# Kernel tuning notes

Hardware: AMD Instinct MI355X
Metric: run time of the kernel (lower is better)

Reference implementation:

```python
import jax, jax.numpy as jnp
import numpy as np

N = 50000      # nodes
E = 800000     # edges (avg degree 16)
IN = 256       # input feature dim
H = 4          # heads
F = 64         # out_feats per head
EF = 64        # edge_feats
NT = 8         # num_etypes
SLOPE = 0.2    # leaky relu negative slope


def setup_inputs() -> dict:
    key = jax.random.key(0)
    ks = jax.random.split(key, 10)
    return {
        "nfeat": jax.random.normal(ks[0], (N, IN), dtype=jnp.float32),
        "fc_w": jax.random.normal(ks[1], (IN, H * F), dtype=jnp.float32) * 0.05,
        "fc_e_w": jax.random.normal(ks[2], (EF, H * EF), dtype=jnp.float32) * 0.05,
        "attn_l": jax.random.normal(ks[3], (H, F), dtype=jnp.float32) * 0.1,
        "attn_r": jax.random.normal(ks[4], (H, F), dtype=jnp.float32) * 0.1,
        "attn_e": jax.random.normal(ks[5], (H, EF), dtype=jnp.float32) * 0.1,
        "edge_emb": jax.random.normal(ks[6], (NT, EF), dtype=jnp.float32),
        "src": jax.random.randint(ks[7], (E,), 0, N, dtype=jnp.int32),
        "dst": jax.random.randint(ks[8], (E,), 0, N, dtype=jnp.int32),
        "etype": jax.random.randint(ks[9], (E,), 0, NT, dtype=jnp.int32),
    }


def reference(nfeat, fc_w, fc_e_w, attn_l, attn_r, attn_e, edge_emb, src, dst, etype):
    # node projection: [N, H, F]
    feat = (nfeat @ fc_w).reshape(N, H, F)
    # per-node attention halves: [N, H]
    el = jnp.einsum("nhf,hf->nh", feat, attn_l)
    er = jnp.einsum("nhf,hf->nh", feat, attn_r)
    # per-etype edge attention term: fc_e(edge_emb).view(NT,H,EF) . attn_e -> [NT, H]
    e_feat = (edge_emb @ fc_e_w).reshape(NT, H, EF)
    ee = jnp.einsum("the,he->th", e_feat, attn_e)
    # raw edge scores: [E, H]
    e = el[src] + er[dst] + ee[etype]
    a_raw = jax.nn.leaky_relu(e, negative_slope=SLOPE)
    # edge_softmax over destination nodes (homogeneous graph -> all edges together)
    seg_max = jax.ops.segment_max(a_raw, dst, num_segments=N)  # [N, H]
    a_exp = jnp.exp(a_raw - seg_max[dst])
    seg_sum = jax.ops.segment_sum(a_exp, dst, num_segments=N)  # [N, H]
    a = a_exp / seg_sum[dst]                                   # [E, H]
    # weighted gather-sum aggregation: sum_e a[e] * feat[src[e]] per dst
    msg = feat[src] * a[:, :, None]                            # [E, H, F]
    rst = jax.ops.segment_sum(msg, dst, num_segments=N)        # [N, H, F]
    return rst, a
```

## Files before the change

kernel.cpp:

```cpp
#include <hip/hip_runtime.h>

#define N_NODES 50000
#define E_EDGES 800000
#define IN_DIM 256
#define H_HEADS 4
#define F_OUT 64
#define EF_DIM 64
#define NT_TYPES 8
#define SLOPE 0.2f
#define HF 256

typedef __attribute__((ext_vector_type(8))) short short8;
typedef __attribute__((ext_vector_type(4))) float f32x4;
typedef unsigned short ushort_t;
typedef unsigned long long u64;

#define FEATBF_OFF 0
#define EL_OFF   6400000
#define ER_OFF   6600000
#define EE_OFF   6800000
#define BT_OFF   6800064
#define INT_OFF  6832832
#define DEG_IOFF     0
#define CURSOR_IOFF  50000
#define RL_IOFF      100000
#define PK_IOFF      150008
#define BO_IOFF      1750008

#define NBLK_GEMM 782
#define NBLK_HIST 3125
#define NCHUNK    196

__device__ __forceinline__ ushort_t f2bf(float f) {
    unsigned u = __float_as_uint(f);
    u += 0x7fffu + ((u >> 16) & 1u);
    return (ushort_t)(u >> 16);
}
__device__ __forceinline__ float bf2f(ushort_t b) {
    return __uint_as_float(((unsigned)b) << 16);
}

__global__ __launch_bounds__(256) void k1_prep(
    const float* __restrict__ edge_emb, const float* __restrict__ fc_e_w,
    const float* __restrict__ attn_e, const float* __restrict__ fc_w,
    float* __restrict__ ee, ushort_t* __restrict__ Bt, int* __restrict__ zero_region)
{
    const int b = blockIdx.x;
    if (b == 0) {
        const int c = threadIdx.x;
        const float ae = attn_e[c];
        const int lane = c & 63, h = c >> 6;
        for (int ty = 0; ty < NT_TYPES; ty++) {
            float v = 0.f;
            #pragma unroll 8
            for (int k = 0; k < EF_DIM; k++)
                v = fmaf(edge_emb[ty * EF_DIM + k], fc_e_w[k * (H_HEADS * EF_DIM) + c], v);
            float contrib = v * ae;
            #pragma unroll
            for (int m = 32; m >= 1; m >>= 1) contrib += __shfl_xor(contrib, m);
            if (lane == 0) ee[ty * H_HEADS + h] = contrib;
        }
    } else if (b <= 256) {
        const int k = b - 1, c = threadIdx.x;
        Bt[(size_t)c * 256 + k] = f2bf(fc_w[(size_t)k * 256 + c]);
    } else {
        const int idx = (b - 257) * 256 + threadIdx.x;
        if (idx < 2 * N_NODES) zero_region[idx] = 0;
    }
}

__global__ __launch_bounds__(256) void k2_hist(
    const int* __restrict__ dst, int* __restrict__ deg)
{
    const int t = blockIdx.x * 256 + threadIdx.x;
    if (t < E_EDGES) atomicAdd(deg + dst[t], 1);
}

__global__ __launch_bounds__(256) void scanA(
    const int* __restrict__ deg, int* __restrict__ rl, int* __restrict__ bo)
{
    __shared__ int sm[256];
    const int c = blockIdx.x, t = threadIdx.x;
    const int g = c * 256 + t;
    const int v = (g < N_NODES) ? deg[g] : 0;
    sm[t] = v;
    __syncthreads();
    int val = v;
    #pragma unroll
    for (int o = 1; o < 256; o <<= 1) {
        int x = (t >= o) ? sm[t - o] : 0;
        __syncthreads();
        val += x;
        sm[t] = val;
        __syncthreads();
    }
    if (g < N_NODES) rl[g] = val - v;
    if (t == 255) bo[c] = val;
}

__global__ __launch_bounds__(256) void scanB(int* __restrict__ bo)
{
    __shared__ int sm[256];
    const int t = threadIdx.x;
    const int v = (t < NCHUNK) ? bo[t] : 0;
    sm[t] = v;
    __syncthreads();
    int val = v;
    #pragma unroll
    for (int o = 1; o < 256; o <<= 1) {
        int x = (t >= o) ? sm[t - o] : 0;
        __syncthreads();
        val += x;
        sm[t] = val;
        __syncthreads();
    }
    if (t < NCHUNK) bo[t] = val - v;
}

__device__ __forceinline__ void gemm_body(
    const float* __restrict__ nfeat, const ushort_t* __restrict__ Bt,
    const float* __restrict__ attn_l, const float* __restrict__ attn_r,
    ushort_t* __restrict__ feat, float* __restrict__ el, float* __restrict__ er,
    int blk)
{
    const int w    = threadIdx.x >> 6;
    const int lane = threadIdx.x & 63;
    const int n16  = lane & 15;
    const int quad = lane >> 4;
    const int row0 = blk * 64;

    f32x4 acc[4][4];
    #pragma unroll
    for (int rt = 0; rt < 4; rt++)
        #pragma unroll
        for (int ct = 0; ct < 4; ct++)
            acc[rt][ct] = (f32x4){0.f, 0.f, 0.f, 0.f};

    for (int kb = 0; kb < IN_DIM; kb += 32) {
        short8 a[4], b[4];
        #pragma unroll
        for (int rt = 0; rt < 4; rt++) {
            int r = row0 + rt * 16 + n16;
            r = r < N_NODES ? r : N_NODES - 1;
            const float* p = nfeat + (size_t)r * IN_DIM + kb + quad * 8;
            const float4 v0 = *(const float4*)p;
            const float4 v1 = *(const float4*)(p + 4);
            short8 t;
            t[0] = (short)f2bf(v0.x); t[1] = (short)f2bf(v0.y);
            t[2] = (short)f2bf(v0.z); t[3] = (short)f2bf(v0.w);
            t[4] = (short)f2bf(v1.x); t[5] = (short)f2bf(v1.y);
            t[6] = (short)f2bf(v1.z); t[7] = (short)f2bf(v1.w);
            a[rt] = t;
        }
        #pragma unroll
        for (int ct = 0; ct < 4; ct++) {
            const int c = w * 64 + ct * 16 + n16;
            b[ct] = *(const short8*)(Bt + (size_t)c * 256 + kb + quad * 8);
        }
        #pragma unroll
        for (int rt = 0; rt < 4; rt++)
            #pragma unroll
            for (int ct = 0; ct < 4; ct++)
                acc[rt][ct] = __builtin_amdgcn_mfma_f32_16x16x32_bf16(a[rt], b[ct], acc[rt][ct], 0, 0, 0);
    }

    float alv[4], arv[4];
    #pragma unroll
    for (int ct = 0; ct < 4; ct++) {
        alv[ct] = attn_l[w * 64 + ct * 16 + n16];
        arv[ct] = attn_r[w * 64 + ct * 16 + n16];
    }
    #pragma unroll
    for (int rt = 0; rt < 4; rt++) {
        #pragma unroll
        for (int reg = 0; reg < 4; reg++) {
            const int row = row0 + rt * 16 + quad * 4 + reg;
            const bool ok = row < N_NODES;
            float pl = 0.f, pr = 0.f;
            #pragma unroll
            for (int ct = 0; ct < 4; ct++) {
                const float v = acc[rt][ct][reg];
                if (ok) feat[(size_t)row * HF + w * 64 + ct * 16 + n16] = f2bf(v);
                pl = fmaf(v, alv[ct], pl);
                pr = fmaf(v, arv[ct], pr);
            }
            #pragma unroll
            for (int m = 8; m >= 1; m >>= 1) {
                pl += __shfl_xor(pl, m);
                pr += __shfl_xor(pr, m);
            }
            if (n16 == 0 && ok) {
                el[row * H_HEADS + w] = pl;
                er[row * H_HEADS + w] = pr;
            }
        }
    }
}

__global__ __launch_bounds__(256) void k4_gemm_scatter(
    const float* __restrict__ nfeat, const ushort_t* __restrict__ Bt,
    const float* __restrict__ attn_l, const float* __restrict__ attn_r,
    ushort_t* __restrict__ feat, float* __restrict__ el, float* __restrict__ er,
    const int* __restrict__ src, const int* __restrict__ dst, const int* __restrict__ etype,
    const int* __restrict__ rl, const int* __restrict__ bo,
    int* __restrict__ cursor, u64* __restrict__ pk)
{
    if (blockIdx.x < NBLK_GEMM) {
        gemm_body(nfeat, Bt, attn_l, attn_r, feat, el, er, blockIdx.x);
    } else {
        const int t = (blockIdx.x - NBLK_GEMM) * 256 + threadIdx.x;
        if (t < E_EDGES) {
            const int d = dst[t];
            const int pos = bo[d >> 8] + rl[d] + atomicAdd(cursor + d, 1);
            pk[pos] = (u64)src[t] | ((u64)etype[t] << 16) | ((u64)t << 32);
        }
    }
}

__global__ __launch_bounds__(256) void agg_kernel(
    const u64* __restrict__ pk, const int* __restrict__ rl, const int* __restrict__ bo,
    const int* __restrict__ degarr,
    const float* __restrict__ el, const float* __restrict__ er,
    const float* __restrict__ ee, const ushort_t* __restrict__ feat,
    float* __restrict__ a_out, float* __restrict__ rst)
{
    const int d = blockIdx.x;
    const int t = threadIdx.x;
    const int h = t >> 6, lane = t & 63;
    const int off = bo[d >> 8] + rl[d];
    const int deg = degarr[d];

    __shared__ int sS[256];
    __shared__ int sE[256];
    __shared__ float sc[4][256];

    if (deg <= 248) {
        const int degP = (deg + 15) & ~15;
        if (t < deg) {
            const u64 p = pk[off + t];
            const int s  = (int)(p & 0xffffu);
            const int ty = (int)((p >> 16) & 0xffu);
            sS[t] = s;
            sE[t] = (int)(p >> 32);
            const float4 el4 = *(const float4*)(el + s * 4);
            const float4 er4 = *(const float4*)(er + d * 4);
            const float4 ee4 = *(const float4*)(ee + ty * 4);
            float v;
            v = el4.x + er4.x + ee4.x; sc[0][t] = v > 0.f ? v : SLOPE * v;
            v = el4.y + er4.y + ee4.y; sc[1][t] = v > 0.f ? v : SLOPE * v;
            v = el4.z + er4.z + ee4.z; sc[2][t] = v > 0.f ? v : SLOPE * v;
            v = el4.w + er4.w + ee4.w; sc[3][t] = v > 0.f ? v : SLOPE * v;
        } else if (t < degP) {
            sS[t] = 0;
            sc[0][t] = 0.f; sc[1][t] = 0.f; sc[2][t] = 0.f; sc[3][t] = 0.f;
        }
        __syncthreads();

        float m = -INFINITY;
        for (int i = lane; i < deg; i += 64) m = fmaxf(m, sc[h][i]);
        #pragma unroll
        for (int w = 32; w >= 1; w >>= 1) m = fmaxf(m, __shfl_xor(m, w));

        float s = 0.f;
        for (int i = lane; i < deg; i += 64) {
            const float e = __expf(sc[h][i] - m);
            sc[h][i] = e;
            s += e;
        }
        #pragma unroll
        for (int w = 32; w >= 1; w >>= 1) s += __shfl_xor(s, w);
        const float inv = 1.f / s;

        for (int i = lane; i < deg; i += 64) {
            const float a = sc[h][i] * inv;
            sc[h][i] = a;
            a_out[sE[i] * 4 + h] = a;
        }
        __syncthreads();

        const int q   = lane >> 4;
        const int l16 = lane & 15;
        const uint2* fb = (const uint2*)feat;
        float a0 = 0.f, a1 = 0.f, a2 = 0.f, a3 = 0.f;
        for (int i = 0; i < degP; i += 16) {
            int sn[4]; float aw[4];
            #pragma unroll
            for (int j = 0; j < 4; j++) {
                const int idx = i + j * 4 + q;
                sn[j] = sS[idx];
                aw[j] = sc[h][idx];
            }
            uint2 u[4];
            #pragma unroll
            for (int j = 0; j < 4; j++)
                u[j] = fb[(size_t)sn[j] * 64 + h * 16 + l16];
            #pragma unroll
            for (int j = 0; j < 4; j++) {
                a0 = fmaf(aw[j], __uint_as_float(u[j].x << 16),          a0);
                a1 = fmaf(aw[j], __uint_as_float(u[j].x & 0xffff0000u),  a1);
                a2 = fmaf(aw[j], __uint_as_float(u[j].y << 16),          a2);
                a3 = fmaf(aw[j], __uint_as_float(u[j].y & 0xffff0000u),  a3);
            }
        }
        a0 += __shfl_xor(a0, 16); a0 += __shfl_xor(a0, 32);
        a1 += __shfl_xor(a1, 16); a1 += __shfl_xor(a1, 32);
        a2 += __shfl_xor(a2, 16); a2 += __shfl_xor(a2, 32);
        a3 += __shfl_xor(a3, 16); a3 += __shfl_xor(a3, 32);
        if (q == 0) {
            float4 o = {a0, a1, a2, a3};
            *(float4*)(rst + (size_t)d * HF + h * 64 + l16 * 4) = o;
        }
    } else {
        const float erh = er[d * 4 + h];
        float m = -INFINITY;
        for (int i = lane; i < deg; i += 64) {
            const u64 p = pk[off + i];
            float v = el[(int)(p & 0xffffu) * 4 + h] + erh + ee[(int)((p >> 16) & 0xffu) * 4 + h];
            v = v > 0.f ? v : SLOPE * v;
            m = fmaxf(m, v);
        }
        #pragma unroll
        for (int w = 32; w >= 1; w >>= 1) m = fmaxf(m, __shfl_xor(m, w));
        float s = 0.f;
        for (int i = lane; i < deg; i += 64) {
            const u64 p = pk[off + i];
            float v = el[(int)(p & 0xffffu) * 4 + h] + erh + ee[(int)((p >> 16) & 0xffu) * 4 + h];
            v = v > 0.f ? v : SLOPE * v;
            s += __expf(v - m);
        }
        #pragma unroll
        for (int w = 32; w >= 1; w >>= 1) s += __shfl_xor(s, w);
        const float inv = 1.f / s;
        float acc = 0.f;
        for (int i = 0; i < deg; i++) {
            const u64 p = pk[off + i];
            const int sn = (int)(p & 0xffffu);
            float v = el[sn * 4 + h] + erh + ee[(int)((p >> 16) & 0xffu) * 4 + h];
            v = v > 0.f ? v : SLOPE * v;
            const float a = __expf(v - m) * inv;
            if (lane == 0) a_out[(int)(p >> 32) * 4 + h] = a;
            acc = fmaf(a, bf2f(feat[(size_t)sn * HF + h * 64 + lane]), acc);
        }
        rst[(size_t)d * HF + h * 64 + lane] = acc;
    }
}

extern "C" void kernel_launch(void* const* d_in, const int* in_sizes, int n_in,
                              void* d_out, int out_size, void* d_ws, size_t ws_size,
                              hipStream_t stream) {
    const float* nfeat    = (const float*)d_in[0];
    const float* fc_w     = (const float*)d_in[1];
    const float* fc_e_w   = (const float*)d_in[2];
    const float* attn_l   = (const float*)d_in[3];
    const float* attn_r   = (const float*)d_in[4];
    const float* attn_e   = (const float*)d_in[5];
    const float* edge_emb = (const float*)d_in[6];
    const int*   src      = (const int*)d_in[7];
    const int*   dst      = (const int*)d_in[8];
    const int*   etype    = (const int*)d_in[9];

    float* ws = (float*)d_ws;
    ushort_t* feat = (ushort_t*)(ws + FEATBF_OFF);
    float* el   = ws + EL_OFF;
    float* er   = ws + ER_OFF;
    float* ee   = ws + EE_OFF;
    ushort_t* Bt = (ushort_t*)(ws + BT_OFF);
    int*   ip      = (int*)(ws + INT_OFF);
    int*   deg     = ip + DEG_IOFF;
    int*   cursor  = ip + CURSOR_IOFF;
    int*   rl      = ip + RL_IOFF;
    u64*   pk      = (u64*)(ip + PK_IOFF);
    int*   bo      = ip + BO_IOFF;

    float* rst   = (float*)d_out;
    float* a_out = (float*)d_out + (size_t)N_NODES * HF;

    k1_prep<<<648, 256, 0, stream>>>(edge_emb, fc_e_w, attn_e, fc_w, ee, Bt, deg);
    k2_hist<<<NBLK_HIST, 256, 0, stream>>>(dst, deg);
    scanA<<<NCHUNK, 256, 0, stream>>>(deg, rl, bo);
    scanB<<<1, 256, 0, stream>>>(bo);
    k4_gemm_scatter<<<NBLK_GEMM + NBLK_HIST, 256, 0, stream>>>(
        nfeat, Bt, attn_l, attn_r, feat, el, er,
        src, dst, etype, rl, bo, cursor, pk);
    agg_kernel<<<N_NODES, 256, 0, stream>>>(pk, rl, bo, deg, el, er, ee, feat, a_out, rst);
}
```

Before: 335.7 us.

## Spread GEMM blocks across CSR-build kernels and use one wave per node in aggregation

The 782 GEMM tiles are split across the histogram, both scan and scatter kernels so projection work overlaps with the serial CSR-building stages. The histogram and scatter now read int4 vectors, handling four edges per thread. Aggregation maps one 64-lane wave per destination node (16 lanes per head) instead of a 256-thread block, and normalisation is deferred to the end. This removes block-level barriers and the idle threads seen at low degree, at the cost of more complex kernel partitioning and LDS use of about 20KB per block.

```diff
diff --git a/kernel.cpp b/kernel.cpp
--- a/kernel.cpp
+++ b/kernel.cpp
@@ -28,8 +28,17 @@
 #define BO_IOFF      1750008
 
 #define NBLK_GEMM 782
-#define NBLK_HIST 3125
+#define NBLK_E4   782
 #define NCHUNK    196
+
+#define G2   312
+#define G3A  120
+#define G3B  100
+#define G4   250
+#define G2_BASE   0
+#define G3A_BASE  312
+#define G3B_BASE  432
+#define G4_BASE   532
 
 __device__ __forceinline__ ushort_t f2bf(float f) {
     unsigned u = __float_as_uint(f);
@@ -69,54 +78,6 @@
     }
 }
 
-__global__ __launch_bounds__(256) void k2_hist(
-    const int* __restrict__ dst, int* __restrict__ deg)
-{
-    const int t = blockIdx.x * 256 + threadIdx.x;
-    if (t < E_EDGES) atomicAdd(deg + dst[t], 1);
-}
-
-__global__ __launch_bounds__(256) void scanA(
-    const int* __restrict__ deg, int* __restrict__ rl, int* __restrict__ bo)
-{
-    __shared__ int sm[256];
-    const int c = blockIdx.x, t = threadIdx.x;
-    const int g = c * 256 + t;
-    const int v = (g < N_NODES) ? deg[g] : 0;
-    sm[t] = v;
-    __syncthreads();
-    int val = v;
-    #pragma unroll
-    for (int o = 1; o < 256; o <<= 1) {
-        int x = (t >= o) ? sm[t - o] : 0;
-        __syncthreads();
-        val += x;
-        sm[t] = val;
-        __syncthreads();
-    }
-    if (g < N_NODES) rl[g] = val - v;
-    if (t == 255) bo[c] = val;
-}
-
-__global__ __launch_bounds__(256) void scanB(int* __restrict__ bo)
-{
-    __shared__ int sm[256];
-    const int t = threadIdx.x;
-    const int v = (t < NCHUNK) ? bo[t] : 0;
-    sm[t] = v;
-    __syncthreads();
-    int val = v;
-    #pragma unroll
-    for (int o = 1; o < 256; o <<= 1) {
-        int x = (t >= o) ? sm[t - o] : 0;
-        __syncthreads();
-        val += x;
-        sm[t] = val;
-        __syncthreads();
-    }
-    if (t < NCHUNK) bo[t] = val - v;
-}
-
 __device__ __forceinline__ void gemm_body(
     const float* __restrict__ nfeat, const ushort_t* __restrict__ Bt,
     const float* __restrict__ attn_l, const float* __restrict__ attn_r,
@@ -197,7 +158,86 @@
     }
 }
 
-__global__ __launch_bounds__(256) void k4_gemm_scatter(
+__global__ __launch_bounds__(256) void k2_hist_gemm(
+    const float* __restrict__ nfeat, const ushort_t* __restrict__ Bt,
+    const float* __restrict__ attn_l, const float* __restrict__ attn_r,
+    ushort_t* __restrict__ feat, float* __restrict__ el, float* __restrict__ er,
+    const int* __restrict__ dst, int* __restrict__ deg)
+{
+    if (blockIdx.x < NBLK_E4) {
+        const int t = blockIdx.x * 256 + threadIdx.x;
+        if (t < E_EDGES / 4) {
+            const int4 d4 = ((const int4*)dst)[t];
+            atomicAdd(deg + d4.x, 1);
+            atomicAdd(deg + d4.y, 1);
+            atomicAdd(deg + d4.z, 1);
+            atomicAdd(deg + d4.w, 1);
+        }
+    } else {
+        gemm_body(nfeat, Bt, attn_l, attn_r, feat, el, er,
+                  G2_BASE + (int)blockIdx.x - NBLK_E4);
+    }
+}
+
+__global__ __launch_bounds__(256) void scanA_gemm(
+    const float* __restrict__ nfeat, const ushort_t* __restrict__ Bt,
+    const float* __restrict__ attn_l, const float* __restrict__ attn_r,
+    ushort_t* __restrict__ feat, float* __restrict__ el, float* __restrict__ er,
+    const int* __restrict__ deg, int* __restrict__ rl, int* __restrict__ bo)
+{
+    if (blockIdx.x < NCHUNK) {
+        __shared__ int sm[256];
+        const int c = blockIdx.x, t = threadIdx.x;
+        const int g = c * 256 + t;
+        const int v = (g < N_NODES) ? deg[g] : 0;
+        sm[t] = v;
+        __syncthreads();
+        int val = v;
+        #pragma unroll
+        for (int o = 1; o < 256; o <<= 1) {
+            int x = (t >= o) ? sm[t - o] : 0;
+            __syncthreads();
+            val += x;
+            sm[t] = val;
+            __syncthreads();
+        }
+        if (g < N_NODES) rl[g] = val - v;
+        if (t == 255) bo[c] = val;
+    } else {
+        gemm_body(nfeat, Bt, attn_l, attn_r, feat, el, er,
+                  G3A_BASE + (int)blockIdx.x - NCHUNK);
+    }
+}
+
+__global__ __launch_bounds__(256) void scanB_gemm(
+    const float* __restrict__ nfeat, const ushort_t* __restrict__ Bt,
+    const float* __restrict__ attn_l, const float* __restrict__ attn_r,
+    ushort_t* __restrict__ feat, float* __restrict__ el, float* __restrict__ er,
+    int* __restrict__ bo)
+{
+    if (blockIdx.x == 0) {
+        __shared__ int sm[256];
+        const int t = threadIdx.x;
+        const int v = (t < NCHUNK) ? bo[t] : 0;
+        sm[t] = v;
+        __syncthreads();
+        int val = v;
+        #pragma unroll
+        for (int o = 1; o < 256; o <<= 1) {
+            int x = (t >= o) ? sm[t - o] : 0;
+            __syncthreads();
+            val += x;
+            sm[t] = val;
+            __syncthreads();
+        }
+        if (t < NCHUNK) bo[t] = val - v;
+    } else {
+        gemm_body(nfeat, Bt, attn_l, attn_r, feat, el, er,
+                  G3B_BASE + (int)blockIdx.x - 1);
+    }
+}
+
+__global__ __launch_bounds__(256) void k4_scatter_gemm(
     const float* __restrict__ nfeat, const ushort_t* __restrict__ Bt,
     const float* __restrict__ attn_l, const float* __restrict__ attn_r,
     ushort_t* __restrict__ feat, float* __restrict__ el, float* __restrict__ er,
@@ -205,15 +245,26 @@
     const int* __restrict__ rl, const int* __restrict__ bo,
     int* __restrict__ cursor, u64* __restrict__ pk)
 {
-    if (blockIdx.x < NBLK_GEMM) {
-        gemm_body(nfeat, Bt, attn_l, attn_r, feat, el, er, blockIdx.x);
-    } else {
-        const int t = (blockIdx.x - NBLK_GEMM) * 256 + threadIdx.x;
-        if (t < E_EDGES) {
-            const int d = dst[t];
-            const int pos = bo[d >> 8] + rl[d] + atomicAdd(cursor + d, 1);
-            pk[pos] = (u64)src[t] | ((u64)etype[t] << 16) | ((u64)t << 32);
-        }
+    if (blockIdx.x < NBLK_E4) {
+        const int t = blockIdx.x * 256 + threadIdx.x;
+        if (t < E_EDGES / 4) {
+            const int4 s4 = ((const int4*)src)[t];
+            const int4 d4 = ((const int4*)dst)[t];
+            const int4 e4 = ((const int4*)etype)[t];
+            const int eb = t * 4;
+            int pos;
+            pos = bo[d4.x >> 8] + rl[d4.x] + atomicAdd(cursor + d4.x, 1);
+            pk[pos] = (u64)s4.x | ((u64)e4.x << 16) | ((u64)(eb + 0) << 32);
+            pos = bo[d4.y >> 8] + rl[d4.y] + atomicAdd(cursor + d4.y, 1);
+            pk[pos] = (u64)s4.y | ((u64)e4.y << 16) | ((u64)(eb + 1) << 32);
+            pos = bo[d4.z >> 8] + rl[d4.z] + atomicAdd(cursor + d4.z, 1);
+            pk[pos] = (u64)s4.z | ((u64)e4.z << 16) | ((u64)(eb + 2) << 32);
+            pos = bo[d4.w >> 8] + rl[d4.w] + atomicAdd(cursor + d4.w, 1);
+            pk[pos] = (u64)s4.w | ((u64)e4.w << 16) | ((u64)(eb + 3) << 32);
+        }
+    } else {
+        gemm_body(nfeat, Bt, attn_l, attn_r, feat, el, er,
+                  G4_BASE + (int)blockIdx.x - NBLK_E4);
     }
 }
 
@@ -224,124 +275,150 @@
     const float* __restrict__ ee, const ushort_t* __restrict__ feat,
     float* __restrict__ a_out, float* __restrict__ rst)
 {
-    const int d = blockIdx.x;
-    const int t = threadIdx.x;
-    const int h = t >> 6, lane = t & 63;
+    const int wid  = threadIdx.x >> 6;
+    const int d    = blockIdx.x * 4 + wid;
+    const int lane = threadIdx.x & 63;
+    const int h    = lane >> 4;
+    const int l    = lane & 15;
+
+    __shared__ __align__(16) ushort_t sS[4][256];
+    __shared__ __align__(16) float    aB[4][256 * 4];
+
+    if (d >= N_NODES) return;
+    ushort_t* sSw = sS[wid];
+    float*    aBw = aB[wid];
+    const uint2* fb = (const uint2*)feat;
+
     const int off = bo[d >> 8] + rl[d];
     const int deg = degarr[d];
-
-    __shared__ int sS[256];
-    __shared__ int sE[256];
-    __shared__ float sc[4][256];
-
-    if (deg <= 248) {
-        const int degP = (deg + 15) & ~15;
-        if (t < deg) {
-            const u64 p = pk[off + t];
-            const int s  = (int)(p & 0xffffu);
-            const int ty = (int)((p >> 16) & 0xffu);
-            sS[t] = s;
-            sE[t] = (int)(p >> 32);
-            const float4 el4 = *(const float4*)(el + s * 4);
-            const float4 er4 = *(const float4*)(er + d * 4);
-            const float4 ee4 = *(const float4*)(ee + ty * 4);
-            float v;
-            v = el4.x + er4.x + ee4.x; sc[0][t] = v > 0.f ? v : SLOPE * v;
-            v = el4.y + er4.y + ee4.y; sc[1][t] = v > 0.f ? v : SLOPE * v;
-            v = el4.z + er4.z + ee4.z; sc[2][t] = v > 0.f ? v : SLOPE * v;
-            v = el4.w + er4.w + ee4.w; sc[3][t] = v > 0.f ? v : SLOPE * v;
-        } else if (t < degP) {
-            sS[t] = 0;
-            sc[0][t] = 0.f; sc[1][t] = 0.f; sc[2][t] = 0.f; sc[3][t] = 0.f;
-        }
-        __syncthreads();
+    const float erh = er[d * 4 + h];
+
+    if (deg <= 256) {
+        const int nch  = (deg + 15) >> 4;
+        const int degP = nch << 4;
 
         float m = -INFINITY;
-        for (int i = lane; i < deg; i += 64) m = fmaxf(m, sc[h][i]);
-        #pragma unroll
-        for (int w = 32; w >= 1; w >>= 1) m = fmaxf(m, __shfl_xor(m, w));
+        for (int c = 0; c < nch; c++) {
+            const int e = c * 16 + l;
+            float v = -INFINITY;
+            if (e < deg) {
+                const u64 p = pk[off + e];
+                const int s  = (int)(p & 0xffffu);
+                const int ty = (int)((p >> 16) & 0xffu);
+                if (h == 0) sSw[e] = (ushort_t)s;
+                v = el[s * 4 + h] + erh + ee[ty * 4 + h];
+                v = v > 0.f ? v : SLOPE * v;
+                aBw[e * 4 + h] = v;
+            }
+            m = fmaxf(m, v);
+        }
+        m = fmaxf(m, __shfl_xor(m, 1));
+        m = fmaxf(m, __shfl_xor(m, 2));
+        m = fmaxf(m, __shfl_xor(m, 4));
+        m = fmaxf(m, __shfl_xor(m, 8));
 
         float s = 0.f;
-        for (int i = lane; i < deg; i += 64) {
-            const float e = __expf(sc[h][i] - m);
-            sc[h][i] = e;
-            s += e;
-        }
-        #pragma unroll
-        for (int w = 32; w >= 1; w >>= 1) s += __shfl_xor(s, w);
-        const float inv = 1.f / s;
-
-        for (int i = lane; i < deg; i += 64) {
-            const float a = sc[h][i] * inv;
-            sc[h][i] = a;
-            a_out[sE[i] * 4 + h] = a;
-        }
-        __syncthreads();
-
-        const int q   = lane >> 4;
-        const int l16 = lane & 15;
-        const uint2* fb = (const uint2*)feat;
-        float a0 = 0.f, a1 = 0.f, a2 = 0.f, a3 = 0.f;
-        for (int i = 0; i < degP; i += 16) {
-            int sn[4]; float aw[4];
+        for (int c = 0; c < nch; c++) {
+            const int e = c * 16 + l;
+            float ev = 0.f;
+            if (e < deg) ev = __expf(aBw[e * 4 + h] - m);
+            else if (h == 0) sSw[e] = 0;
+            aBw[e * 4 + h] = ev;
+            s += ev;
+        }
+        s += __shfl_xor(s, 1);
+        s += __shfl_xor(s, 2);
+        s += __shfl_xor(s, 4);
+        s += __shfl_xor(s, 8);
+        const float inv = (deg > 0) ? 1.f / s : 0.f;
+
+        asm volatile("s_waitcnt lgkmcnt(0)" ::: "memory");
+
+        const float inv0 = __shfl(inv, 0);
+        const float inv1 = __shfl(inv, 16);
+        const float inv2 = __shfl(inv, 32);
+        const float inv3 = __shfl(inv, 48);
+
+        if (h == 0) {
+            for (int c = 0; c < nch; c++) {
+                const int e = c * 16 + l;
+                if (e < deg) {
+                    const u64 p = pk[off + e];
+                    const int eid = (int)(p >> 32);
+                    const float4 t = *(const float4*)(aBw + e * 4);
+                    float4 av;
+                    av.x = t.x * inv0;
+                    av.y = t.y * inv1;
+                    av.z = t.z * inv2;
+                    av.w = t.w * inv3;
+                    *(float4*)(a_out + (size_t)eid * 4) = av;
+                }
+            }
+        }
+
+        float4 acc = {0.f, 0.f, 0.f, 0.f};
+        const int col = h * 16 + l;
+        for (int e0 = 0; e0 < degP; e0 += 4) {
             #pragma unroll
             for (int j = 0; j < 4; j++) {
-                const int idx = i + j * 4 + q;
-                sn[j] = sS[idx];
-                aw[j] = sc[h][idx];
-            }
-            uint2 u[4];
-            #pragma unroll
-            for (int j = 0; j < 4; j++)
-                u[j] = fb[(size_t)sn[j] * 64 + h * 16 + l16];
-            #pragma unroll
-            for (int j = 0; j < 4; j++) {
-                a0 = fmaf(aw[j], __uint_as_float(u[j].x << 16),          a0);
-                a1 = fmaf(aw[j], __uint_as_float(u[j].x & 0xffff0000u),  a1);
-                a2 = fmaf(aw[j], __uint_as_float(u[j].y << 16),          a2);
-                a3 = fmaf(aw[j], __uint_as_float(u[j].y & 0xffff0000u),  a3);
-            }
-        }
-        a0 += __shfl_xor(a0, 16); a0 += __shfl_xor(a0, 32);
-        a1 += __shfl_xor(a1, 16); a1 += __shfl_xor(a1, 32);
-        a2 += __shfl_xor(a2, 16); a2 += __shfl_xor(a2, 32);
-        a3 += __shfl_xor(a3, 16); a3 += __shfl_xor(a3, 32);
-        if (q == 0) {
-            float4 o = {a0, a1, a2, a3};
-            *(float4*)(rst + (size_t)d * HF + h * 64 + l16 * 4) = o;
-        }
-    } else {
-        const float erh = er[d * 4 + h];
+                const int e = e0 + j;
+                const int sn = (int)sSw[e];
+                const float aw = aBw[e * 4 + h];
+                const uint2 u = fb[(size_t)sn * 64 + col];
+                acc.x = fmaf(aw, __uint_as_float(u.x << 16),         acc.x);
+                acc.y = fmaf(aw, __uint_as_float(u.x & 0xffff0000u), acc.y);
+                acc.z = fmaf(aw, __uint_as_float(u.y << 16),         acc.z);
+                acc.w = fmaf(aw, __uint_as_float(u.y & 0xffff0000u), acc.w);
+            }
+        }
+        acc.x *= inv; acc.y *= inv; acc.z *= inv; acc.w *= inv;
+        *(float4*)(rst + (size_t)d * HF + h * 64 + l * 4) = acc;
+    } else {
         float m = -INFINITY;
-        for (int i = lane; i < deg; i += 64) {
+        for (int i = l; i < deg; i += 16) {
             const u64 p = pk[off + i];
             float v = el[(int)(p & 0xffffu) * 4 + h] + erh + ee[(int)((p >> 16) & 0xffu) * 4 + h];
             v = v > 0.f ? v : SLOPE * v;
             m = fmaxf(m, v);
         }
-        #pragma unroll
-        for (int w = 32; w >= 1; w >>= 1) m = fmaxf(m, __shfl_xor(m, w));
+        m = fmaxf(m, __shfl_xor(m, 1));
+        m = fmaxf(m, __shfl_xor(m, 2));
+        m = fmaxf(m, __shfl_xor(m, 4));
+        m = fmaxf(m, __shfl_xor(m, 8));
         float s = 0.f;
-        for (int i = lane; i < deg; i += 64) {
+        for (int i = l; i < deg; i += 16) {
             const u64 p = pk[off + i];
             float v = el[(int)(p & 0xffffu) * 4 + h] + erh + ee[(int)((p >> 16) & 0xffu) * 4 + h];
             v = v > 0.f ? v : SLOPE * v;
             s += __expf(v - m);
         }
-        #pragma unroll
-        for (int w = 32; w >= 1; w >>= 1) s += __shfl_xor(s, w);
+        s += __shfl_xor(s, 1);
+        s += __shfl_xor(s, 2);
+        s += __shfl_xor(s, 4);
+        s += __shfl_xor(s, 8);
         const float inv = 1.f / s;
-        float acc = 0.f;
-        for (int i = 0; i < deg; i++) {
+        for (int i = l; i < deg; i += 16) {
             const u64 p = pk[off + i];
             const int sn = (int)(p & 0xffffu);
             float v = el[sn * 4 + h] + erh + ee[(int)((p >> 16) & 0xffu) * 4 + h];
             v = v > 0.f ? v : SLOPE * v;
-            const float a = __expf(v - m) * inv;
-            if (lane == 0) a_out[(int)(p >> 32) * 4 + h] = a;
-            acc = fmaf(a, bf2f(feat[(size_t)sn * HF + h * 64 + lane]), acc);
-        }
-        rst[(size_t)d * HF + h * 64 + lane] = acc;
+            a_out[(int)(p >> 32) * 4 + h] = __expf(v - m) * inv;
+        }
+        float4 acc = {0.f, 0.f, 0.f, 0.f};
+        const int col = h * 16 + l;
+        for (int e = 0; e < deg; e++) {
+            const u64 p = pk[off + e];
+            const int sn = (int)(p & 0xffffu);
+            float v = el[sn * 4 + h] + erh + ee[(int)((p >> 16) & 0xffu) * 4 + h];
+            v = v > 0.f ? v : SLOPE * v;
+            const float aw = __expf(v - m) * inv;
+            const uint2 u = fb[(size_t)sn * 64 + col];
+            acc.x = fmaf(aw, __uint_as_float(u.x << 16),         acc.x);
+            acc.y = fmaf(aw, __uint_as_float(u.x & 0xffff0000u), acc.y);
+            acc.z = fmaf(aw, __uint_as_float(u.y << 16),         acc.z);
+            acc.w = fmaf(aw, __uint_as_float(u.y & 0xffff0000u), acc.w);
+        }
+        *(float4*)(rst + (size_t)d * HF + h * 64 + l * 4) = acc;
     }
 }
 
@@ -376,11 +453,15 @@
     float* a_out = (float*)d_out + (size_t)N_NODES * HF;
 
     k1_prep<<<648, 256, 0, stream>>>(edge_emb, fc_e_w, attn_e, fc_w, ee, Bt, deg);
-    k2_hist<<<NBLK_HIST, 256, 0, stream>>>(dst, deg);
-    scanA<<<NCHUNK, 256, 0, stream>>>(deg, rl, bo);
-    scanB<<<1, 256, 0, stream>>>(bo);
-    k4_gemm_scatter<<<NBLK_GEMM + NBLK_HIST, 256, 0, stream>>>(
+    k2_hist_gemm<<<NBLK_E4 + G2, 256, 0, stream>>>(
+        nfeat, Bt, attn_l, attn_r, feat, el, er, dst, deg);
+    scanA_gemm<<<NCHUNK + G3A, 256, 0, stream>>>(
+        nfeat, Bt, attn_l, attn_r, feat, el, er, deg, rl, bo);
+    scanB_gemm<<<1 + G3B, 256, 0, stream>>>(
+        nfeat, Bt, attn_l, attn_r, feat, el, er, bo);
+    k4_scatter_gemm<<<NBLK_E4 + G4, 256, 0, stream>>>(
         nfeat, Bt, attn_l, attn_r, feat, el, er,
         src, dst, etype, rl, bo, cursor, pk);
-    agg_kernel<<<N_NODES, 256, 0, stream>>>(pk, rl, bo, deg, el, er, ee, feat, a_out, rst);
-}
+    agg_kernel<<<(N_NODES + 3) / 4, 256, 0, stream>>>(
+        pk, rl, bo, deg, el, er, ee, feat, a_out, rst);
+}
```

New measurement: 373.8 us. 11.3% more time.
